# Optimization experiments

Hardware: AMD Instinct MI355X
Metric: run time of the kernel (lower is better)

## Reference

```python
import jax, jax.numpy as jnp
import numpy as np

N_NODES = 2048
EMBED = 256
STATE = 128
HID = 256
N_ACT = 256
TEAMS = 8
PAIR_F = 14


def setup_inputs() -> dict:
    key = jax.random.key(0)
    ks = jax.random.split(key, 12)
    B, T = 16, 32
    node_embeddings = jax.random.normal(ks[0], (N_NODES, EMBED), jnp.float32)
    states = jax.random.normal(ks[1], (B, T, STATE), jnp.float32)
    pair_features = jax.random.normal(ks[2], (B, T, N_ACT, PAIR_F), jnp.float32)
    proc_action_indices = jax.random.randint(ks[3], (N_ACT,), 0, N_NODES)
    in_dim = EMBED * 4 + PAIR_F
    s = lambda k, sh, fan: jax.random.normal(k, sh, jnp.float32) / np.sqrt(fan)
    return {
        "node_embeddings": node_embeddings,
        "states": states,
        "pair_features": pair_features,
        "proc_action_indices": proc_action_indices,
        "team_table": jax.random.normal(ks[4], (TEAMS, EMBED), jnp.float32),
        "Ws": s(ks[5], (STATE, EMBED), STATE),
        "bs": jnp.zeros((EMBED,), jnp.float32),
        "W1": s(ks[6], (in_dim, HID), in_dim),
        "b1": jnp.zeros((HID,), jnp.float32),
        "W2": s(ks[7], (HID, HID), HID),
        "b2": jnp.zeros((HID,), jnp.float32),
        "W3": s(ks[8], (HID, 1), HID),
        "b3": jnp.zeros((1,), jnp.float32),
    }


def reference(node_embeddings, states, pair_features, proc_action_indices,
              team_table, Ws, bs, W1, b1, W2, b2, W3, b3):
    B, T, A, F = pair_features.shape
    team_ids = jnp.arange(A) % TEAMS  # registered buffer
    # [A, E] gathered / per-action embeddings
    proc_emb = node_embeddings[proc_action_indices]          # [A, E]
    team_emb = team_table[team_ids]                          # [A, E]
    global_emb = jnp.mean(node_embeddings, axis=0)           # [E]
    state_emb = jax.nn.relu(states @ Ws + bs)                # [B, T, E]
    # broadcast + concat -> [B, T, A, 4E + F]
    bT = (B, T, A)
    scorer_input = jnp.concatenate([
        jnp.broadcast_to(proc_emb[None, None], bT + (proc_emb.shape[-1],)),
        jnp.broadcast_to(team_emb[None, None], bT + (team_emb.shape[-1],)),
        jnp.broadcast_to(global_emb[None, None, None], bT + (global_emb.shape[-1],)),
        jnp.broadcast_to(state_emb[:, :, None], bT + (state_emb.shape[-1],)),
        pair_features,
    ], axis=-1)
    h = jax.nn.relu(scorer_input @ W1 + b1)
    h = jax.nn.relu(h @ W2 + b2)
    scores = (h @ W3 + b3)[..., 0]  # [B, T, A]
    return scores[:, :, None, :]    # [B, T, 1, A]
```

## Files before the change

### kernel.cpp

```cpp
#include <hip/hip_runtime.h>
#include <hip/hip_bf16.h>

#define N_NODES 2048
#define EMBED 256
#define STATE 128
#define HID 256
#define N_ACT 256
#define TEAMS 8
#define PAIR_F 14
#define BT_TOTAL 512
#define M_TOTAL (BT_TOTAL * N_ACT)

typedef _Float16 f16_t;
typedef _Float16 f16x8 __attribute__((ext_vector_type(8)));
typedef _Float16 f16x4 __attribute__((ext_vector_type(4)));
typedef _Float16 f16x2 __attribute__((ext_vector_type(2)));
typedef float f32x4 __attribute__((ext_vector_type(4)));

__device__ __forceinline__ size_t reord_idx(int k, int n, int KB) {
    return (size_t)(((n >> 4) * KB + (k >> 5)) * 4 + ((k >> 3) & 3)) * 128 +
           (size_t)(n & 15) * 8 + (k & 7);
}

__device__ __forceinline__ size_t par_idx(int a, int n) {
    return (size_t)(a >> 4) * 4096 + (size_t)(n >> 2) * 64 + (a & 15) * 4 + (n & 3);
}

__device__ __forceinline__ f16x8 gather8(const float* __restrict__ W, int k0, int n, int ld) {
    f16x8 r;
#pragma unroll
    for (int j = 0; j < 8; ++j) r[j] = (f16_t)W[(size_t)(k0 + j) * ld + n];
    return r;
}

__device__ __forceinline__ f16x2 pk_relu(f16x2 x) {
    f16x2 r;
    asm("v_pk_max_f16 %0, %1, %2" : "=v"(r) : "v"(x), "v"(f16x2{(_Float16)0, (_Float16)0}));
    return r;
}

__device__ __forceinline__ f16x2 cvt_pk(float lo, float hi) {
    return __builtin_bit_cast(f16x2, __builtin_amdgcn_cvt_pkrtz(lo, hi));
}

__global__ void k_prep(const float* __restrict__ ne, const int* __restrict__ idx,
                       const float* __restrict__ team, const float* __restrict__ states,
                       const float* __restrict__ Ws, const float* __restrict__ W1,
                       const float* __restrict__ W2, float* __restrict__ gpart,
                       f16_t* __restrict__ vecs, f16_t* __restrict__ W1abT,
                       f16_t* __restrict__ W1cT, f16_t* __restrict__ W1dT,
                       f16_t* __restrict__ WsT, f16_t* __restrict__ W2s,
                       f16_t* __restrict__ w1pt, f16_t* __restrict__ states_h) {
    int bid = blockIdx.x;
    if (bid < 64) {
        int t = threadIdx.x;
        float s = 0.f;
        const float* base = ne + (size_t)bid * 32 * EMBED + t;
#pragma unroll
        for (int i = 0; i < 32; ++i) s += base[(size_t)i * EMBED];
        gpart[bid * EMBED + t] = s;
        return;
    }
    int u = (bid - 64) * 256 + threadIdx.x;
    if (u < 16384) {
        int a = u >> 6, e = (u & 63) * 8;
        f16x8 r;
        if (e < 256) {
            const float* src = ne + (size_t)idx[a] * EMBED + e;
#pragma unroll
            for (int j = 0; j < 8; ++j) r[j] = (f16_t)src[j];
        } else {
            const float* src = team + (size_t)(a % TEAMS) * EMBED + (e - 256);
#pragma unroll
            for (int j = 0; j < 8; ++j) r[j] = (f16_t)src[j];
        }
        *(f16x8*)(vecs + (size_t)u * 8) = r;
        return;
    }
    u -= 16384;
    if (u < 16384) {
        int c = u & 15, q = (u >> 4) & 3, kb = (u >> 6) & 15, g = u >> 10;
        *(f16x8*)(W1abT + (size_t)u * 8) = gather8(W1, kb * 32 + q * 8, g * 16 + c, HID);
        return;
    }
    u -= 16384;
    if (u < 8192) {
        int c = u & 15, q = (u >> 4) & 3, kb = (u >> 6) & 7, g = u >> 9;
        *(f16x8*)(W1cT + (size_t)u * 8) = gather8(W1, 512 + kb * 32 + q * 8, g * 16 + c, HID);
        return;
    }
    u -= 8192;
    if (u < 8192) {
        int c = u & 15, q = (u >> 4) & 3, kb = (u >> 6) & 7, g = u >> 9;
        *(f16x8*)(W1dT + (size_t)u * 8) = gather8(W1, 768 + kb * 32 + q * 8, g * 16 + c, HID);
        return;
    }
    u -= 8192;
    if (u < 4096) {
        int c = u & 15, q = (u >> 4) & 3, kb = (u >> 6) & 3, g = u >> 8;
        *(f16x8*)(WsT + (size_t)u * 8) = gather8(Ws, kb * 32 + q * 8, g * 16 + c, EMBED);
        return;
    }
    u -= 4096;
    if (u < 8192) {
        int c = u & 15, q = (u >> 4) & 3, kb = (u >> 6) & 7, g = u >> 9;
        *(f16x8*)(W2s + (size_t)u * 8) = gather8(W2, kb * 32 + q * 8, g * 16 + c, HID);
        return;
    }
    u -= 8192;
    if (u < 1024) {
        int c = u & 15, q = (u >> 4) & 3, g = u >> 6;
        int n = g * 16 + c, k0 = q * 8;
        f16x8 r;
#pragma unroll
        for (int j = 0; j < 8; ++j) {
            int k = k0 + j;
            r[j] = (f16_t)((k < PAIR_F) ? W1[(size_t)(1024 + k) * HID + n] : 0.f);
        }
        *(f16x8*)(w1pt + (size_t)u * 8) = r;
        return;
    }
    u -= 1024;
    if (u < 8192) {
        const float* src = states + (size_t)u * 8;
        f16x8 r;
#pragma unroll
        for (int j = 0; j < 8; ++j) r[j] = (f16_t)src[j];
        *(f16x8*)(states_h + (size_t)u * 8) = r;
    }
}

__global__ __launch_bounds__(256, 4) void k_pp(
    const f16_t* __restrict__ states_h, const f16_t* __restrict__ WsT,
    const float* __restrict__ bs, const f16_t* __restrict__ W1dT,
    const f16_t* __restrict__ vecs, const f16_t* __restrict__ W1abT,
    const f16_t* __restrict__ W1cT, const float* __restrict__ gpart,
    const float* __restrict__ b1, f16_t* __restrict__ paR,
    f16_t* __restrict__ pbt_h) {
    __shared__ __align__(16) f16_t se[64 * 256];
    __shared__ __align__(16) f16_t gml[256];
    const int tid = threadIdx.x;
    const int wid = tid >> 6, lane = tid & 63;
    const int c = lane & 15, q = lane >> 4;
    int bid = blockIdx.x;

    if (bid >= 8) {
        {
            float s = 0.f;
#pragma unroll 8
            for (int p = 0; p < 64; ++p) s += gpart[p * EMBED + tid];
            gml[tid] = (f16_t)(s * (1.0f / N_NODES));
        }
        __syncthreads();
        int b = bid - 8;
        const int m0 = (b >> 2) * 64, n0 = (b & 3) * 64;
        const int n = n0 + wid * 16 + c;
        const int g = n >> 4;
        f32x4 acc[4] = {f32x4{0,0,0,0}, f32x4{0,0,0,0}, f32x4{0,0,0,0}, f32x4{0,0,0,0}};
        for (int ks = 0; ks < 16; ++ks) {
            f16x8 bf = *(const f16x8*)(W1abT + (size_t)((g * 16 + ks) * 4 + q) * 128 + c * 8);
#pragma unroll
            for (int mi = 0; mi < 4; ++mi) {
                f16x8 af = *(const f16x8*)(vecs + (size_t)(m0 + mi * 16 + c) * 512 + ks * 32 + q * 8);
                acc[mi] = __builtin_amdgcn_mfma_f32_16x16x32_f16(af, bf, acc[mi], 0, 0, 0);
            }
        }
#pragma unroll
        for (int ks = 0; ks < 8; ++ks) {
            f16x8 bf = *(const f16x8*)(W1cT + (size_t)((g * 8 + ks) * 4 + q) * 128 + c * 8);
            f16x8 af = *(const f16x8*)(gml + ks * 32 + q * 8);
#pragma unroll
            for (int mi = 0; mi < 4; ++mi)
                acc[mi] = __builtin_amdgcn_mfma_f32_16x16x32_f16(af, bf, acc[mi], 0, 0, 0);
        }
        float b1v = b1[n];
#pragma unroll
        for (int mi = 0; mi < 4; ++mi)
#pragma unroll
            for (int j = 0; j < 4; ++j) {
                int a = m0 + mi * 16 + q * 4 + j;
                paR[par_idx(a, n)] = (f16_t)(acc[mi][j] + b1v);
            }
        return;
    }

    const int bt0 = bid * 64;
    f32x4 acc[4][4];
#pragma unroll
    for (int mi = 0; mi < 4; ++mi)
#pragma unroll
        for (int ni = 0; ni < 4; ++ni) acc[mi][ni] = f32x4{0, 0, 0, 0};
#pragma unroll
    for (int ks = 0; ks < 4; ++ks) {
        f16x8 bh[4];
#pragma unroll
        for (int ni = 0; ni < 4; ++ni) {
            int g = wid * 4 + ni;
            bh[ni] = *(const f16x8*)(WsT + (size_t)((g * 4 + ks) * 4 + q) * 128 + c * 8);
        }
#pragma unroll
        for (int mi = 0; mi < 4; ++mi) {
            f16x8 af = *(const f16x8*)(states_h + (size_t)(bt0 + mi * 16 + c) * STATE + ks * 32 + q * 8);
#pragma unroll
            for (int ni = 0; ni < 4; ++ni)
                acc[mi][ni] = __builtin_amdgcn_mfma_f32_16x16x32_f16(af, bh[ni], acc[mi][ni], 0, 0, 0);
        }
    }
#pragma unroll
    for (int mi = 0; mi < 4; ++mi)
#pragma unroll
        for (int ni = 0; ni < 4; ++ni) {
            float bsv = bs[wid * 64 + ni * 16 + c];
#pragma unroll
            for (int j = 0; j < 4; ++j) {
                int m = mi * 16 + q * 4 + j;
                int n = wid * 64 + ni * 16 + c;
                se[m * 256 + (n ^ ((m & 7) << 3))] = (f16_t)fmaxf(acc[mi][ni][j] + bsv, 0.f);
            }
        }
#pragma unroll
    for (int mi = 0; mi < 4; ++mi)
#pragma unroll
        for (int ni = 0; ni < 4; ++ni) acc[mi][ni] = f32x4{0, 0, 0, 0};
    __syncthreads();
#pragma unroll
    for (int ks = 0; ks < 8; ++ks) {
        f16x8 bh[4];
#pragma unroll
        for (int ni = 0; ni < 4; ++ni) {
            int g = wid * 4 + ni;
            bh[ni] = *(const f16x8*)(W1dT + (size_t)((g * 8 + ks) * 4 + q) * 128 + c * 8);
        }
#pragma unroll
        for (int mi = 0; mi < 4; ++mi) {
            int m = mi * 16 + c;
            f16x8 ah = *(const f16x8*)(&se[m * 256 + ((ks * 32 + q * 8) ^ ((m & 7) << 3))]);
#pragma unroll
            for (int ni = 0; ni < 4; ++ni)
                acc[mi][ni] = __builtin_amdgcn_mfma_f32_16x16x32_f16(ah, bh[ni], acc[mi][ni], 0, 0, 0);
        }
    }
#pragma unroll
    for (int mi = 0; mi < 4; ++mi)
#pragma unroll
        for (int ni = 0; ni < 4; ++ni)
#pragma unroll
            for (int j = 0; j < 4; ++j)
                pbt_h[(size_t)(bt0 + mi * 16 + q * 4 + j) * HID + wid * 64 + ni * 16 + c] =
                    (f16_t)acc[mi][ni][j];
}

__global__ __launch_bounds__(512, 4) void k_main(
    const float* __restrict__ pf, const f16_t* __restrict__ paR,
    const f16_t* __restrict__ pbt, const f16_t* __restrict__ w2s,
    const f16_t* __restrict__ w1pt, const float* __restrict__ b2,
    const float* __restrict__ W3, const float* __restrict__ b3,
    float* __restrict__ out) {
    __shared__ __align__(16) f16_t Ah[128 * 256];
    __shared__ __align__(16) f16_t pfs16[128 * 16];
    __shared__ float red[4][128];

    const int tid = threadIdx.x;
    const int wid = tid >> 6, lane = tid & 63;
    const int wr = wid >> 2, wc = wid & 3;
    const int c = lane & 15, q = lane >> 4;

    const int r0 = blockIdx.x * 128;
    const int bt = r0 >> 8;
    const int a0 = r0 & 255;

    if (tid < 448) {
        const float4 v = ((const float4*)(pf + (size_t)r0 * PAIR_F))[tid];
        float vv[4] = {v.x, v.y, v.z, v.w};
        int f = tid * 4;
#pragma unroll
        for (int i = 0; i < 4; ++i) {
            int e = f + i;
            int m = e / PAIR_F, k = e - m * PAIR_F;
            pfs16[m * 16 + k] = (f16_t)vv[i];
        }
    } else {
        int t2 = tid - 448;
        *(f16x2*)(pfs16 + (t2 * 2) * 16 + 14) = f16x2{(_Float16)0, (_Float16)0};
        *(f16x2*)(pfs16 + (t2 * 2 + 1) * 16 + 14) = f16x2{(_Float16)0, (_Float16)0};
    }

    f32x4 acc[16];
#pragma unroll
    for (int i = 0; i < 16; ++i) acc[i] = f32x4{0, 0, 0, 0};

    f16x8 af[4];
#pragma unroll
    for (int nf = 0; nf < 4; ++nf) {
        int g = wc * 4 + nf;
        af[nf] = *(const f16x8*)(w1pt + (size_t)(g * 4 + q) * 128 + c * 8);
    }

    __syncthreads();

#pragma unroll
    for (int mf = 0; mf < 4; ++mf) {
        int m = wr * 64 + mf * 16 + c;
        f16x8 bf;
        if (q < 2) bf = *(const f16x8*)(pfs16 + m * 16 + q * 8);
        else bf = f16x8{(_Float16)0, (_Float16)0, (_Float16)0, (_Float16)0,
                        (_Float16)0, (_Float16)0, (_Float16)0, (_Float16)0};
#pragma unroll
        for (int nf = 0; nf < 4; ++nf)
            acc[nf * 4 + mf] = __builtin_amdgcn_mfma_f32_16x16x32_f16(af[nf], bf, acc[nf * 4 + mf], 0, 0, 0);
    }

#pragma unroll
    for (int nf = 0; nf < 4; ++nf) {
        int n0 = wc * 64 + nf * 16 + q * 4;
        f16x4 pbtv = *(const f16x4*)(pbt + (size_t)bt * HID + n0);
        f16x2 pb01 = {pbtv[0], pbtv[1]}, pb23 = {pbtv[2], pbtv[3]};
#pragma unroll
        for (int mf = 0; mf < 4; ++mf) {
            int m = wr * 64 + mf * 16 + c;
            f16x4 pav = *(const f16x4*)(paR + (size_t)((a0 >> 4) + wr * 4 + mf) * 4096 +
                                        (size_t)(n0 >> 2) * 64 + c * 4);
            f16x2 pa01 = {pav[0], pav[1]}, pa23 = {pav[2], pav[3]};
            f32x4 a = acc[nf * 4 + mf];
            f16x2 h01 = cvt_pk(a[0], a[1]);
            f16x2 h23 = cvt_pk(a[2], a[3]);
            h01 = pk_relu(h01 + pa01 + pb01);
            h23 = pk_relu(h23 + pa23 + pb23);
            f16x4 hv = __builtin_shufflevector(h01, h23, 0, 1, 2, 3);
            *(f16x4*)(&Ah[m * 256 + (n0 ^ ((m & 7) << 3))]) = hv;
        }
    }

#pragma unroll
    for (int i = 0; i < 16; ++i) acc[i] = f32x4{0, 0, 0, 0};

    f16x8 bh[4];
#pragma unroll
    for (int ni = 0; ni < 4; ++ni) {
        int g = wc * 4 + ni;
        bh[ni] = *(const f16x8*)(w2s + (size_t)((g * 8 + 0) * 4 + q) * 128 + c * 8);
    }

    __syncthreads();

#pragma unroll
    for (int ks = 0; ks < 8; ++ks) {
        f16x8 bhn[4];
        if (ks < 7) {
#pragma unroll
            for (int ni = 0; ni < 4; ++ni) {
                int g = wc * 4 + ni;
                bhn[ni] = *(const f16x8*)(w2s + (size_t)((g * 8 + ks + 1) * 4 + q) * 128 + c * 8);
            }
        }
#pragma unroll
        for (int mi = 0; mi < 4; ++mi) {
            int m = wr * 64 + mi * 16 + c;
            int kx = (ks * 32 + q * 8) ^ ((m & 7) << 3);
            f16x8 ah = *(const f16x8*)(&Ah[m * 256 + kx]);
#pragma unroll
            for (int ni = 0; ni < 4; ++ni)
                acc[mi * 4 + ni] = __builtin_amdgcn_mfma_f32_16x16x32_f16(ah, bh[ni], acc[mi * 4 + ni], 0, 0, 0);
        }
#pragma unroll
        for (int ni = 0; ni < 4; ++ni) bh[ni] = bhn[ni];
    }

    float p[4][4];
#pragma unroll
    for (int mi = 0; mi < 4; ++mi)
#pragma unroll
        for (int j = 0; j < 4; ++j) p[mi][j] = 0.f;
#pragma unroll
    for (int ni = 0; ni < 4; ++ni) {
        int n = wc * 64 + ni * 16 + c;
        float b2v = b2[n];
        float w3v = W3[n];
#pragma unroll
        for (int mi = 0; mi < 4; ++mi)
#pragma unroll
            for (int j = 0; j < 4; ++j)
                p[mi][j] = fmaf(fmaxf(acc[mi * 4 + ni][j] + b2v, 0.f), w3v, p[mi][j]);
    }
#pragma unroll
    for (int off = 1; off < 16; off <<= 1)
#pragma unroll
        for (int mi = 0; mi < 4; ++mi)
#pragma unroll
            for (int j = 0; j < 4; ++j) p[mi][j] += __shfl_xor(p[mi][j], off, 64);

    if (c == 0) {
#pragma unroll
        for (int mi = 0; mi < 4; ++mi)
#pragma unroll
            for (int j = 0; j < 4; ++j) red[wc][wr * 64 + mi * 16 + q * 4 + j] = p[mi][j];
    }
    __syncthreads();

    if (tid < 128) {
        out[(size_t)r0 + tid] = red[0][tid] + red[1][tid] + red[2][tid] + red[3][tid] + b3[0];
    }
}

extern "C" void kernel_launch(void* const* d_in, const int* in_sizes, int n_in,
                              void* d_out, int out_size, void* d_ws, size_t ws_size,
                              hipStream_t stream) {
    (void)in_sizes; (void)n_in; (void)out_size; (void)ws_size;
    const float* ne     = (const float*)d_in[0];
    const float* states = (const float*)d_in[1];
    const float* pf     = (const float*)d_in[2];
    const int*   idx    = (const int*)d_in[3];
    const float* team   = (const float*)d_in[4];
    const float* Ws     = (const float*)d_in[5];
    const float* bs     = (const float*)d_in[6];
    const float* W1     = (const float*)d_in[7];
    const float* b1     = (const float*)d_in[8];
    const float* W2     = (const float*)d_in[9];
    const float* b2     = (const float*)d_in[10];
    const float* W3     = (const float*)d_in[11];
    const float* b3     = (const float*)d_in[12];
    float* out = (float*)d_out;

    char* ws = (char*)d_ws;
    float* gpart    = (float*)(ws + 0);
    f16_t* vecs     = (f16_t*)(ws + 65536);
    f16_t* W1abT    = (f16_t*)(ws + 327680);
    f16_t* W1cT     = (f16_t*)(ws + 589824);
    f16_t* W1dT     = (f16_t*)(ws + 720896);
    f16_t* WsT      = (f16_t*)(ws + 851968);
    f16_t* W2s      = (f16_t*)(ws + 917504);
    f16_t* w1pt     = (f16_t*)(ws + 1048576);
    f16_t* states_h = (f16_t*)(ws + 1064960);
    f16_t* paR      = (f16_t*)(ws + 1196032);
    f16_t* pbt_h    = (f16_t*)(ws + 1327104);

    k_prep<<<64 + 276, 256, 0, stream>>>(ne, idx, team, states, Ws, W1, W2, gpart,
                                         vecs, W1abT, W1cT, W1dT, WsT, W2s, w1pt,
                                         states_h);
    k_pp<<<24, 256, 0, stream>>>(states_h, WsT, bs, W1dT, vecs, W1abT, W1cT,
                                 gpart, b1, paR, pbt_h);
    k_main<<<M_TOTAL / 128, 512, 0, stream>>>(pf, paR, pbt_h, W2s, w1pt, b2, W3, b3, out);
}
```

Before: 47.80 us.

## Pre-convert pair features to padded fp16 in prep kernel and halve k_pp tiles

Moves the fp32-to-fp16 conversion and 16-wide padding of pair_features out of k_main into a new section of k_prep, so k_main reads fragments straight from global memory with no shared staging buffer and no block barrier. It also halves the per-block tile in k_pp (32 rows instead of 64), doubling its grid to use more CUs. The trade-off is an extra round trip through global memory for the pair features (fp32 read plus fp16 write, then a second read) and a larger prep launch.

```diff
diff --git a/kernel.cpp b/kernel.cpp
--- a/kernel.cpp
+++ b/kernel.cpp
@@ -46,11 +46,12 @@
 __global__ void k_prep(const float* __restrict__ ne, const int* __restrict__ idx,
                        const float* __restrict__ team, const float* __restrict__ states,
                        const float* __restrict__ Ws, const float* __restrict__ W1,
-                       const float* __restrict__ W2, float* __restrict__ gpart,
-                       f16_t* __restrict__ vecs, f16_t* __restrict__ W1abT,
-                       f16_t* __restrict__ W1cT, f16_t* __restrict__ W1dT,
-                       f16_t* __restrict__ WsT, f16_t* __restrict__ W2s,
-                       f16_t* __restrict__ w1pt, f16_t* __restrict__ states_h) {
+                       const float* __restrict__ W2, const float* __restrict__ pf,
+                       float* __restrict__ gpart, f16_t* __restrict__ vecs,
+                       f16_t* __restrict__ W1abT, f16_t* __restrict__ W1cT,
+                       f16_t* __restrict__ W1dT, f16_t* __restrict__ WsT,
+                       f16_t* __restrict__ W2s, f16_t* __restrict__ w1pt,
+                       f16_t* __restrict__ states_h, f16_t* __restrict__ pf16) {
     int bid = blockIdx.x;
     if (bid < 64) {
         int t = threadIdx.x;
@@ -127,6 +128,28 @@
 #pragma unroll
         for (int j = 0; j < 8; ++j) r[j] = (f16_t)src[j];
         *(f16x8*)(states_h + (size_t)u * 8) = r;
+        return;
+    }
+    u -= 8192;
+    if (u < 262144) {
+        int m = u >> 1, h = u & 1;
+        const float* row = pf + (size_t)m * PAIR_F;
+        f16x8 r;
+        if (h == 0) {
+#pragma unroll
+            for (int j = 0; j < 4; ++j) {
+                float2 v = *(const float2*)(row + j * 2);
+                r[j * 2] = (f16_t)v.x; r[j * 2 + 1] = (f16_t)v.y;
+            }
+        } else {
+#pragma unroll
+            for (int j = 0; j < 3; ++j) {
+                float2 v = *(const float2*)(row + 8 + j * 2);
+                r[j * 2] = (f16_t)v.x; r[j * 2 + 1] = (f16_t)v.y;
+            }
+            r[6] = (f16_t)0.f; r[7] = (f16_t)0.f;
+        }
+        *(f16x8*)(pf16 + (size_t)u * 8) = r;
     }
 }
 
@@ -137,14 +160,14 @@
     const f16_t* __restrict__ W1cT, const float* __restrict__ gpart,
     const float* __restrict__ b1, f16_t* __restrict__ paR,
     f16_t* __restrict__ pbt_h) {
-    __shared__ __align__(16) f16_t se[64 * 256];
+    __shared__ __align__(16) f16_t se[32 * 256];
     __shared__ __align__(16) f16_t gml[256];
     const int tid = threadIdx.x;
     const int wid = tid >> 6, lane = tid & 63;
     const int c = lane & 15, q = lane >> 4;
     int bid = blockIdx.x;
 
-    if (bid >= 8) {
+    if (bid >= 16) {
         {
             float s = 0.f;
 #pragma unroll 8
@@ -152,15 +175,15 @@
             gml[tid] = (f16_t)(s * (1.0f / N_NODES));
         }
         __syncthreads();
-        int b = bid - 8;
-        const int m0 = (b >> 2) * 64, n0 = (b & 3) * 64;
+        int b = bid - 16;
+        const int m0 = (b >> 2) * 32, n0 = (b & 3) * 64;
         const int n = n0 + wid * 16 + c;
         const int g = n >> 4;
-        f32x4 acc[4] = {f32x4{0,0,0,0}, f32x4{0,0,0,0}, f32x4{0,0,0,0}, f32x4{0,0,0,0}};
+        f32x4 acc[2] = {f32x4{0,0,0,0}, f32x4{0,0,0,0}};
         for (int ks = 0; ks < 16; ++ks) {
             f16x8 bf = *(const f16x8*)(W1abT + (size_t)((g * 16 + ks) * 4 + q) * 128 + c * 8);
 #pragma unroll
-            for (int mi = 0; mi < 4; ++mi) {
+            for (int mi = 0; mi < 2; ++mi) {
                 f16x8 af = *(const f16x8*)(vecs + (size_t)(m0 + mi * 16 + c) * 512 + ks * 32 + q * 8);
                 acc[mi] = __builtin_amdgcn_mfma_f32_16x16x32_f16(af, bf, acc[mi], 0, 0, 0);
             }
@@ -170,12 +193,12 @@
             f16x8 bf = *(const f16x8*)(W1cT + (size_t)((g * 8 + ks) * 4 + q) * 128 + c * 8);
             f16x8 af = *(const f16x8*)(gml + ks * 32 + q * 8);
 #pragma unroll
-            for (int mi = 0; mi < 4; ++mi)
+            for (int mi = 0; mi < 2; ++mi)
                 acc[mi] = __builtin_amdgcn_mfma_f32_16x16x32_f16(af, bf, acc[mi], 0, 0, 0);
         }
         float b1v = b1[n];
 #pragma unroll
-        for (int mi = 0; mi < 4; ++mi)
+        for (int mi = 0; mi < 2; ++mi)
 #pragma unroll
             for (int j = 0; j < 4; ++j) {
                 int a = m0 + mi * 16 + q * 4 + j;
@@ -184,10 +207,10 @@
         return;
     }
 
-    const int bt0 = bid * 64;
-    f32x4 acc[4][4];
-#pragma unroll
-    for (int mi = 0; mi < 4; ++mi)
+    const int bt0 = bid * 32;
+    f32x4 acc[2][4];
+#pragma unroll
+    for (int mi = 0; mi < 2; ++mi)
 #pragma unroll
         for (int ni = 0; ni < 4; ++ni) acc[mi][ni] = f32x4{0, 0, 0, 0};
 #pragma unroll
@@ -199,7 +222,7 @@
             bh[ni] = *(const f16x8*)(WsT + (size_t)((g * 4 + ks) * 4 + q) * 128 + c * 8);
         }
 #pragma unroll
-        for (int mi = 0; mi < 4; ++mi) {
+        for (int mi = 0; mi < 2; ++mi) {
             f16x8 af = *(const f16x8*)(states_h + (size_t)(bt0 + mi * 16 + c) * STATE + ks * 32 + q * 8);
 #pragma unroll
             for (int ni = 0; ni < 4; ++ni)
@@ -207,7 +230,7 @@
         }
     }
 #pragma unroll
-    for (int mi = 0; mi < 4; ++mi)
+    for (int mi = 0; mi < 2; ++mi)
 #pragma unroll
         for (int ni = 0; ni < 4; ++ni) {
             float bsv = bs[wid * 64 + ni * 16 + c];
@@ -219,7 +242,7 @@
             }
         }
 #pragma unroll
-    for (int mi = 0; mi < 4; ++mi)
+    for (int mi = 0; mi < 2; ++mi)
 #pragma unroll
         for (int ni = 0; ni < 4; ++ni) acc[mi][ni] = f32x4{0, 0, 0, 0};
     __syncthreads();
@@ -232,7 +255,7 @@
             bh[ni] = *(const f16x8*)(W1dT + (size_t)((g * 8 + ks) * 4 + q) * 128 + c * 8);
         }
 #pragma unroll
-        for (int mi = 0; mi < 4; ++mi) {
+        for (int mi = 0; mi < 2; ++mi) {
             int m = mi * 16 + c;
             f16x8 ah = *(const f16x8*)(&se[m * 256 + ((ks * 32 + q * 8) ^ ((m & 7) << 3))]);
 #pragma unroll
@@ -241,7 +264,7 @@
         }
     }
 #pragma unroll
-    for (int mi = 0; mi < 4; ++mi)
+    for (int mi = 0; mi < 2; ++mi)
 #pragma unroll
         for (int ni = 0; ni < 4; ++ni)
 #pragma unroll
@@ -251,13 +274,12 @@
 }
 
 __global__ __launch_bounds__(512, 4) void k_main(
-    const float* __restrict__ pf, const f16_t* __restrict__ paR,
+    const f16_t* __restrict__ pf16, const f16_t* __restrict__ paR,
     const f16_t* __restrict__ pbt, const f16_t* __restrict__ w2s,
     const f16_t* __restrict__ w1pt, const float* __restrict__ b2,
     const float* __restrict__ W3, const float* __restrict__ b3,
     float* __restrict__ out) {
     __shared__ __align__(16) f16_t Ah[128 * 256];
-    __shared__ __align__(16) f16_t pfs16[128 * 16];
     __shared__ float red[4][128];
 
     const int tid = threadIdx.x;
@@ -269,22 +291,6 @@
     const int bt = r0 >> 8;
     const int a0 = r0 & 255;
 
-    if (tid < 448) {
-        const float4 v = ((const float4*)(pf + (size_t)r0 * PAIR_F))[tid];
-        float vv[4] = {v.x, v.y, v.z, v.w};
-        int f = tid * 4;
-#pragma unroll
-        for (int i = 0; i < 4; ++i) {
-            int e = f + i;
-            int m = e / PAIR_F, k = e - m * PAIR_F;
-            pfs16[m * 16 + k] = (f16_t)vv[i];
-        }
-    } else {
-        int t2 = tid - 448;
-        *(f16x2*)(pfs16 + (t2 * 2) * 16 + 14) = f16x2{(_Float16)0, (_Float16)0};
-        *(f16x2*)(pfs16 + (t2 * 2 + 1) * 16 + 14) = f16x2{(_Float16)0, (_Float16)0};
-    }
-
     f32x4 acc[16];
 #pragma unroll
     for (int i = 0; i < 16; ++i) acc[i] = f32x4{0, 0, 0, 0};
@@ -296,13 +302,11 @@
         af[nf] = *(const f16x8*)(w1pt + (size_t)(g * 4 + q) * 128 + c * 8);
     }
 
-    __syncthreads();
-
 #pragma unroll
     for (int mf = 0; mf < 4; ++mf) {
         int m = wr * 64 + mf * 16 + c;
         f16x8 bf;
-        if (q < 2) bf = *(const f16x8*)(pfs16 + m * 16 + q * 8);
+        if (q < 2) bf = *(const f16x8*)(pf16 + (size_t)(r0 + m) * 16 + q * 8);
         else bf = f16x8{(_Float16)0, (_Float16)0, (_Float16)0, (_Float16)0,
                         (_Float16)0, (_Float16)0, (_Float16)0, (_Float16)0};
 #pragma unroll
@@ -433,11 +437,12 @@
     f16_t* states_h = (f16_t*)(ws + 1064960);
     f16_t* paR      = (f16_t*)(ws + 1196032);
     f16_t* pbt_h    = (f16_t*)(ws + 1327104);
-
-    k_prep<<<64 + 276, 256, 0, stream>>>(ne, idx, team, states, Ws, W1, W2, gpart,
-                                         vecs, W1abT, W1cT, W1dT, WsT, W2s, w1pt,
-                                         states_h);
-    k_pp<<<24, 256, 0, stream>>>(states_h, WsT, bs, W1dT, vecs, W1abT, W1cT,
+    f16_t* pf16     = (f16_t*)(ws + 1589248);
+
+    k_prep<<<64 + 1300, 256, 0, stream>>>(ne, idx, team, states, Ws, W1, W2, pf,
+                                          gpart, vecs, W1abT, W1cT, W1dT, WsT, W2s,
+                                          w1pt, states_h, pf16);
+    k_pp<<<48, 256, 0, stream>>>(states_h, WsT, bs, W1dT, vecs, W1abT, W1cT,
                                  gpart, b1, paR, pbt_h);
-    k_main<<<M_TOTAL / 128, 512, 0, stream>>>(pf, paR, pbt_h, W2s, w1pt, b2, W3, b3, out);
-}
+    k_main<<<M_TOTAL / 128, 512, 0, stream>>>(pf16, paR, pbt_h, W2s, w1pt, b2, W3, b3, out);
+}
```

Result: faster. 43.21 us (-9.6%).
